# Performance work log

Hardware: AMD Instinct MI355X
Metric: run time of the kernel (lower is better)

The kernel has to match this reference:

```python
import jax, jax.numpy as jnp
import numpy as np

B, T, H, M, S, E, IN = 8, 2048, 64, 32, 20, 3, 32
EPS = 1e-8  # torch CosineSimilarity eps


def setup_inputs() -> dict:
    key = jax.random.key(0)
    ks = jax.random.split(key, 7)
    return {
        "x": jax.random.normal(ks[0], (B, T, IN), jnp.float32),
        "hidden": jax.random.normal(ks[1], (E, B, T, H), jnp.float32),
        "memory": jax.random.normal(ks[2], (S, M), jnp.float32),
        "Wq": jax.random.normal(ks[3], (E, H, M), jnp.float32),
        "Wk": jax.random.normal(ks[4], (E, H, M), jnp.float32),
        "Wv": jax.random.normal(ks[5], (E, H, M), jnp.float32),
        "input_query": jax.random.normal(ks[6], (IN, M), jnp.float32),
    }


def _cosine(a, b):
    # torch.nn.CosineSimilarity(dim=-1): each vector norm clamped to eps
    na = jnp.maximum(jnp.linalg.norm(a, axis=-1), EPS)
    nb = jnp.maximum(jnp.linalg.norm(b, axis=-1), EPS)
    return jnp.sum(a * b, axis=-1) / (na * nb)


def reference(x, hidden, memory, Wq, Wk, Wv, input_query):
    # query_mem: soft read from global memory slots
    q_in = jnp.einsum('bti,im->btm', x, input_query)           # [B,T,M]
    mem_sc = jax.nn.softmax(jnp.einsum('btm,sm->bts', q_in, memory), axis=-1)
    memories = jnp.einsum('bts,sm->btm', mem_sc, memory)       # [B,T,M]

    # per-expert tiny self-attention (vectorized over expert axis e)
    Q = jnp.einsum('ebth,ehm->ebtm', hidden, Wq)
    K = jnp.einsum('ebth,ehm->ebtm', hidden, Wk)
    V = jnp.einsum('ebth,ehm->ebtm', hidden, Wv)
    energy = jnp.einsum('ebtm,ebsm->ebts', Q, K)               # [E,B,T,T]
    att = jax.nn.softmax(energy, axis=-1)
    out = jnp.einsum('ebts,ebsm->ebtm', att, V)                # [E,B,T,M]

    cos = _cosine(memories[None], out)                         # [E,B,T]
    return jnp.moveaxis(cos, 0, -1)                            # [B,T,E]
```

## Files before the change

kernel.cpp:

```cpp
#include <hip/hip_runtime.h>
#include <hip/hip_bf16.h>

#define Bv  8
#define Tv  2048
#define Hv  64
#define Mv  32
#define Sv  20
#define Ev  3
#define INv 32
#define LOG2E 1.44269504088896340736f

typedef __attribute__((ext_vector_type(8))) _Float16 half8;
typedef __attribute__((ext_vector_type(2))) __fp16 fp16x2;
typedef __attribute__((ext_vector_type(4))) float float4v;

__global__ __launch_bounds__(256) void qkv_kernel(
    const float* __restrict__ hidden,
    const float* __restrict__ Wq,
    const float* __restrict__ Wk,
    const float* __restrict__ Wv,
    const float* __restrict__ x,
    const float* __restrict__ memory,
    const float* __restrict__ iq,
    _Float16* __restrict__ Qh, _Float16* __restrict__ Ql,
    _Float16* __restrict__ Kh, _Float16* __restrict__ Kl,
    _Float16* __restrict__ Vth,
    float* __restrict__ memout)
{
    __shared__ __align__(16) char qsm[43008];
    __shared__ float sIQ[32][32];
    __shared__ float sM[20][32];
    float* sHT = (float*)qsm;
    float* sW  = (float*)(qsm + 17408);

    int bid  = blockIdx.x;
    int tile = bid & 31;
    int b    = (bid >> 5) & 7;
    int e    = bid >> 8;
    int tid  = threadIdx.x;
    size_t eb = (size_t)(e * Bv + b);
    size_t row0 = eb * Tv + (size_t)tile * 64;
    const float* hbase = hidden + row0 * Hv;

    for (int i = tid; i < 32 * 32; i += 256) sIQ[i >> 5][i & 31] = iq[i];
    for (int i = tid; i < 20 * 32; i += 256) sM[i >> 5][i & 31] = memory[i];

    {
        int r  = tid >> 2;
        int c4 = tid & 3;
#pragma unroll
        for (int hh = 0; hh < 4; ++hh) {
            int h4 = c4 + hh * 4;
            float4 v = ((const float4*)(hbase + (size_t)r * Hv))[h4];
            sHT[(h4*4+0)*68 + r] = v.x; sHT[(h4*4+1)*68 + r] = v.y;
            sHT[(h4*4+2)*68 + r] = v.z; sHT[(h4*4+3)*68 + r] = v.w;
        }
    }
    {
        const float* wq = Wq + (size_t)e * Hv * Mv;
        const float* wk = Wk + (size_t)e * Hv * Mv;
        const float* wv = Wv + (size_t)e * Hv * Mv;
        for (int i = tid; i < Hv * Mv; i += 256) {
            int h = i >> 5, m = i & 31;
            sW[h*100 + m]      = wq[i];
            sW[h*100 + 32 + m] = wk[i];
            sW[h*100 + 64 + m] = wv[i];
        }
    }
    __syncthreads();

    int ty = tid >> 4, tx = tid & 15;
    float acc[4][6];
#pragma unroll
    for (int i = 0; i < 4; ++i)
#pragma unroll
        for (int j = 0; j < 6; ++j) acc[i][j] = 0.f;

    for (int h = 0; h < 64; ++h) {
        float4 av = *(const float4*)&sHT[h*68 + ty * 4];
        float a[4] = {av.x, av.y, av.z, av.w};
        float bb[6];
#pragma unroll
        for (int j = 0; j < 6; ++j) bb[j] = sW[h*100 + tx * 6 + j];
#pragma unroll
        for (int i = 0; i < 4; ++i)
#pragma unroll
            for (int j = 0; j < 6; ++j) acc[i][j] = fmaf(a[i], bb[j], acc[i][j]);
    }

    __syncthreads();
    char* sQh = qsm;
    char* sQl = qsm + 4096;
    char* sKh = qsm + 8192;
    char* sKl = qsm + 12288;
    char* sVh = qsm + 16384;
#pragma unroll
    for (int i = 0; i < 4; ++i) {
        int row = ty * 4 + i;
#pragma unroll
        for (int j = 0; j < 6; ++j) {
            int c = tx * 6 + j;
            float v = acc[i][j];
            if (c < 32) {
                v *= LOG2E;
                _Float16 h16 = (_Float16)v;
                _Float16 l16 = (_Float16)(v - (float)h16);
                *(_Float16*)(sQh + row * 64 + c * 2) = h16;
                *(_Float16*)(sQl + row * 64 + c * 2) = l16;
            } else if (c < 64) {
                _Float16 h16 = (_Float16)v;
                _Float16 l16 = (_Float16)(v - (float)h16);
                int m = c - 32, q = m >> 3, wi = m & 7;
                int off = row * 64 + (((q + row) & 3) << 4) + wi * 2;
                *(_Float16*)(sKh + off) = h16;
                *(_Float16*)(sKl + off) = l16;
            } else {
                int d = c - 64, c8 = row >> 3, wi = row & 7;
                int off = d * 128 + (((c8 + d) & 7) << 4) + wi * 2;
                *(_Float16*)(sVh + off) = (_Float16)v;
            }
        }
    }
    __syncthreads();

    size_t pb = eb * (size_t)Tv * 32 + (size_t)tile * 2048;
    _Float16* dsts[5] = {Qh + pb, Ql + pb, Kh + pb, Kl + pb, Vth + pb};
#pragma unroll
    for (int pl = 0; pl < 5; ++pl)
        ((float4*)dsts[pl])[tid] = ((const float4*)(qsm + pl * 4096))[tid];

    if (e == 0 && tid < 64) {
        int t = b * Tv + tile * 64 + tid;
        const float4* xr = (const float4*)(x + (size_t)t * INv);
        float xv[32];
#pragma unroll
        for (int i = 0; i < 8; ++i) {
            float4 v = xr[i];
            xv[4*i] = v.x; xv[4*i+1] = v.y; xv[4*i+2] = v.z; xv[4*i+3] = v.w;
        }
        float qm[32];
#pragma unroll
        for (int m = 0; m < 32; ++m) qm[m] = 0.f;
        for (int i = 0; i < 32; ++i) {
            float xi = xv[i];
#pragma unroll
            for (int m4 = 0; m4 < 8; ++m4) {
                float4 wv = *(const float4*)&sIQ[i][m4 * 4];
                qm[4*m4]   = fmaf(xi, wv.x, qm[4*m4]);
                qm[4*m4+1] = fmaf(xi, wv.y, qm[4*m4+1]);
                qm[4*m4+2] = fmaf(xi, wv.z, qm[4*m4+2]);
                qm[4*m4+3] = fmaf(xi, wv.w, qm[4*m4+3]);
            }
        }
        float sc[20];
#pragma unroll
        for (int j = 0; j < 20; ++j) {
            float a2 = 0.f;
#pragma unroll
            for (int m = 0; m < 32; ++m) a2 = fmaf(qm[m], sM[j][m], a2);
            sc[j] = a2;
        }
        float mx = sc[0];
#pragma unroll
        for (int j = 1; j < 20; ++j) mx = fmaxf(mx, sc[j]);
        float psum = 0.f, p[20];
#pragma unroll
        for (int j = 0; j < 20; ++j) { p[j] = exp2f((sc[j] - mx) * LOG2E); psum += p[j]; }
        float inv = 1.0f / psum;
        float mo[32];
#pragma unroll
        for (int m = 0; m < 32; ++m) mo[m] = 0.f;
        for (int j = 0; j < 20; ++j) {
            float pj = p[j];
#pragma unroll
            for (int m = 0; m < 32; ++m) mo[m] = fmaf(pj, sM[j][m], mo[m]);
        }
        float4* outp = (float4*)(memout + (size_t)t * Mv);
#pragma unroll
        for (int m4 = 0; m4 < 8; ++m4) {
            float4 v;
            v.x = mo[4*m4] * inv; v.y = mo[4*m4+1] * inv;
            v.z = mo[4*m4+2] * inv; v.w = mo[4*m4+3] * inv;
            outp[m4] = v;
        }
    }
}

__device__ __forceinline__ void load_lds16(const _Float16* g, char* l) {
    __builtin_amdgcn_global_load_lds(
        (const __attribute__((address_space(1))) void*)g,
        (__attribute__((address_space(3))) void*)l, 16, 0, 0);
}

__global__ __launch_bounds__(256, 1) void attn_kernel(
    const _Float16* __restrict__ Qh, const _Float16* __restrict__ Ql,
    const _Float16* __restrict__ Kh, const _Float16* __restrict__ Kl,
    const _Float16* __restrict__ Vth,
    const float* __restrict__ memv,
    float* __restrict__ out)
{
    __shared__ __align__(16) char smem[32768];
    const int PW = 24576;

    int bid  = blockIdx.x;
    int xcd  = bid & 7;
    int slot = bid >> 3;
    int tile = slot & 31;
    int ebi  = xcd + ((slot >> 5) << 3);
    int e    = ebi >> 3;
    int b    = ebi & 7;
    int tid  = threadIdx.x;
    int lane = tid & 63;
    int w    = tid >> 6;
    int quad = lane >> 4;
    int l15  = lane & 15;
    size_t eb = (size_t)ebi;
    int q0 = tile * 64 + w * 16;

    size_t qoff = (eb * Tv + (size_t)(q0 + l15)) * 32 + quad * 8;
    half8 qH = *(const half8*)(Qh + qoff);
    half8 qL = *(const half8*)(Ql + qoff);

    float4v O0 = {0.f, 0.f, 0.f, 0.f};
    float4v O1 = {0.f, 0.f, 0.f, 0.f};
    float m_run = -3.0e38f;

    size_t ebOff = eb * (size_t)Tv * 32;
    const _Float16* gp[3] = {Kh + ebOff, Kl + ebOff, Vth + ebOff};

#pragma unroll
    for (int j = 0; j < 3; ++j) {
        int idx = w * 3 + j, p = idx >> 2, k = idx & 3;
        load_lds16(gp[p] + (size_t)k * 512 + lane * 8,
                   smem + p * 4096 + k * 1024);
    }

    for (int c = 0; c < 32; ++c) {
        int pb = c & 1;
        __syncthreads();
        if (c + 1 < 32) {
#pragma unroll
            for (int j = 0; j < 3; ++j) {
                int idx = w * 3 + j, p = idx >> 2, k = idx & 3;
                load_lds16(gp[p] + (size_t)(c + 1) * 2048 + k * 512 + lane * 8,
                           smem + (pb ^ 1) * 12288 + p * 4096 + k * 1024);
            }
        }
        const char* base = smem + pb * 12288;

        float s[16];
        float cmax = -3.0e38f;
#pragma unroll
        for (int tau = 0; tau < 4; ++tau) {
            int r = tau * 16 + l15;
            int sw = ((quad + r) & 3) << 4;
            half8 aH = *(const half8*)(base + r * 64 + sw);
            half8 aL = *(const half8*)(base + 4096 + r * 64 + sw);
            float4v acc = {0.f, 0.f, 0.f, 0.f};
            acc = __builtin_amdgcn_mfma_f32_16x16x32_f16(aH, qL, acc, 0, 0, 0);
            acc = __builtin_amdgcn_mfma_f32_16x16x32_f16(aL, qH, acc, 0, 0, 0);
            acc = __builtin_amdgcn_mfma_f32_16x16x32_f16(aH, qH, acc, 0, 0, 0);
#pragma unroll
            for (int r2 = 0; r2 < 4; ++r2) {
                s[tau * 4 + r2] = acc[r2];
                cmax = fmaxf(cmax, acc[r2]);
            }
        }
        cmax = fmaxf(cmax, __shfl_xor(cmax, 16));
        cmax = fmaxf(cmax, __shfl_xor(cmax, 32));
        float mNew  = fmaxf(m_run, cmax);
        float alpha = exp2f(m_run - mNew);
#pragma unroll
        for (int i = 0; i < 16; ++i)
            s[i] = exp2f(s[i] - mNew);
        m_run = mNew;

#pragma unroll
        for (int r = 0; r < 4; ++r) {
            float ar = __shfl(alpha, quad * 4 + r, 16);
            O0[r] *= ar;
            O1[r] *= ar;
        }

        char* pw = smem + PW + w * 2048 + l15 * 128;
        int xr = l15 & 7;
#pragma unroll
        for (int tau = 0; tau < 4; ++tau) {
            fp16x2 h01 = __builtin_amdgcn_cvt_pkrtz(s[tau*4+0], s[tau*4+1]);
            fp16x2 h23 = __builtin_amdgcn_cvt_pkrtz(s[tau*4+2], s[tau*4+3]);
            uint2 u;
            u.x = __builtin_bit_cast(unsigned int, h01);
            u.y = __builtin_bit_cast(unsigned int, h23);
            int bi = tau * 2 + (quad >> 1);
            *(uint2*)(pw + ((bi ^ xr) << 4) + (quad & 1) * 8) = u;
        }
        __asm__ volatile("" ::: "memory");

#pragma unroll
        for (int ks = 0; ks < 2; ++ks) {
            int swv = ((ks * 4 + quad + l15) & 7) << 4;
            half8 pA  = *(const half8*)(pw + (((ks * 4 + quad) ^ xr) << 4));
            half8 v0H = *(const half8*)(base + 8192 + l15 * 128 + swv);
            half8 v1H = *(const half8*)(base + 8192 + (16 + l15) * 128 + swv);
            O0 = __builtin_amdgcn_mfma_f32_16x16x32_f16(pA, v0H, O0, 0, 0, 0);
            O1 = __builtin_amdgcn_mfma_f32_16x16x32_f16(pA, v1H, O1, 0, 0, 0);
        }
    }

    const float* mb = memv + (size_t)b * Tv * 32;
    float dotr[4], nor[4], nmr[4];
#pragma unroll
    for (int r = 0; r < 4; ++r) {
        int trow = q0 + quad * 4 + r;
        float mv0 = mb[(size_t)trow * 32 + l15];
        float mv1 = mb[(size_t)trow * 32 + 16 + l15];
        float d  = O0[r] * mv0 + O1[r] * mv1;
        float n  = O0[r] * O0[r] + O1[r] * O1[r];
        float nm = mv0 * mv0 + mv1 * mv1;
#pragma unroll
        for (int delta = 1; delta < 16; delta <<= 1) {
            d  += __shfl_xor(d,  delta);
            n  += __shfl_xor(n,  delta);
            nm += __shfl_xor(nm, delta);
        }
        dotr[r] = d; nor[r] = n; nmr[r] = nm;
    }
    if (l15 < 4) {
        int r = l15;
        float na = fmaxf(sqrtf(nmr[r]), 1e-8f);
        float nb = fmaxf(sqrtf(nor[r]), 1e-30f);
        float cosv = dotr[r] / (na * nb);
        int trow = q0 + quad * 4 + r;
        out[((size_t)b * Tv + trow) * Ev + e] = cosv;
    }
}

extern "C" void kernel_launch(void* const* d_in, const int* in_sizes, int n_in,
                              void* d_out, int out_size, void* d_ws, size_t ws_size,
                              hipStream_t stream) {
    const float* x      = (const float*)d_in[0];
    const float* hidden = (const float*)d_in[1];
    const float* memory = (const float*)d_in[2];
    const float* Wq     = (const float*)d_in[3];
    const float* Wk     = (const float*)d_in[4];
    const float* Wv     = (const float*)d_in[5];
    const float* iq     = (const float*)d_in[6];
    float* out          = (float*)d_out;

    char* ws = (char*)d_ws;
    const size_t PLANE = (size_t)Ev * Bv * Tv * 32 * 2;
    float*    memout = (float*)ws;
    _Float16* Qh  = (_Float16*)(ws + 2097152);
    _Float16* Ql  = (_Float16*)(ws + 2097152 + PLANE);
    _Float16* Kh  = (_Float16*)(ws + 2097152 + 2 * PLANE);
    _Float16* Kl  = (_Float16*)(ws + 2097152 + 3 * PLANE);
    _Float16* Vth = (_Float16*)(ws + 2097152 + 4 * PLANE);

    qkv_kernel<<<Ev * Bv * (Tv / 64), 256, 0, stream>>>(hidden, Wq, Wk, Wv,
                                                        x, memory, iq,
                                                        Qh, Ql, Kh, Kl, Vth, memout);
    attn_kernel<<<Ev * Bv * (Tv / 64), 256, 0, stream>>>(Qh, Ql, Kh, Kl, Vth,
                                                         memout, out);
}
```

Measured before the change: 148.6 us.

## Compute QKV projection with split-fp16 MFMA instead of scalar FMA

Replaces the scalar FP32 FMA loop in the QKV projection kernel with MFMA 16x16x32 fp16 instructions. Both the hidden rows and the weights are split into hi/lo fp16 parts, and three MFMAs per k-block approximate FP32 precision. Weights are pre-split into swizzled shared memory, the hidden transpose through LDS is removed, and the LOG2E scale is folded into the weights. It also loads the iq/memory tables only for expert 0 blocks. This shrinks shared memory and cuts ALU work in the projection stage, but it drops the lo*lo term, which adds small rounding error.

```diff
diff --git a/kernel.cpp b/kernel.cpp
--- a/kernel.cpp
+++ b/kernel.cpp
@@ -13,6 +13,16 @@
 typedef __attribute__((ext_vector_type(8))) _Float16 half8;
 typedef __attribute__((ext_vector_type(2))) __fp16 fp16x2;
 typedef __attribute__((ext_vector_type(4))) float float4v;
+
+__device__ __forceinline__ void split2x4(float4 a, float4 b, half8& h, half8& l) {
+    float vv[8] = {a.x, a.y, a.z, a.w, b.x, b.y, b.z, b.w};
+#pragma unroll
+    for (int i = 0; i < 8; ++i) {
+        _Float16 hh = (_Float16)vv[i];
+        h[i] = hh;
+        l[i] = (_Float16)(vv[i] - (float)hh);
+    }
+}
 
 __global__ __launch_bounds__(256) void qkv_kernel(
     const float* __restrict__ hidden,
@@ -27,93 +37,108 @@
     _Float16* __restrict__ Vth,
     float* __restrict__ memout)
 {
-    __shared__ __align__(16) char qsm[43008];
+    __shared__ __align__(16) char sBlob[24576];
     __shared__ float sIQ[32][32];
     __shared__ float sM[20][32];
-    float* sHT = (float*)qsm;
-    float* sW  = (float*)(qsm + 17408);
 
     int bid  = blockIdx.x;
     int tile = bid & 31;
     int b    = (bid >> 5) & 7;
     int e    = bid >> 8;
     int tid  = threadIdx.x;
+    int lane = tid & 63;
+    int w    = tid >> 6;
+    int quad = lane >> 4;
+    int l15  = lane & 15;
     size_t eb = (size_t)(e * Bv + b);
     size_t row0 = eb * Tv + (size_t)tile * 64;
     const float* hbase = hidden + row0 * Hv;
 
-    for (int i = tid; i < 32 * 32; i += 256) sIQ[i >> 5][i & 31] = iq[i];
-    for (int i = tid; i < 20 * 32; i += 256) sM[i >> 5][i & 31] = memory[i];
+    const float* arow = hbase + (size_t)(w * 16 + l15) * Hv + quad * 8;
+    float4 a0 = *(const float4*)(arow);
+    float4 a1 = *(const float4*)(arow + 4);
+    float4 a2 = *(const float4*)(arow + 32);
+    float4 a3 = *(const float4*)(arow + 36);
+
+    if (e == 0) {
+        for (int i = tid; i < 32 * 32; i += 256) sIQ[i >> 5][i & 31] = iq[i];
+        for (int i = tid; i < 20 * 32; i += 256) sM[i >> 5][i & 31] = memory[i];
+    }
 
     {
-        int r  = tid >> 2;
-        int c4 = tid & 3;
-#pragma unroll
-        for (int hh = 0; hh < 4; ++hh) {
-            int h4 = c4 + hh * 4;
-            float4 v = ((const float4*)(hbase + (size_t)r * Hv))[h4];
-            sHT[(h4*4+0)*68 + r] = v.x; sHT[(h4*4+1)*68 + r] = v.y;
-            sHT[(h4*4+2)*68 + r] = v.z; sHT[(h4*4+3)*68 + r] = v.w;
-        }
-    }
-    {
-        const float* wq = Wq + (size_t)e * Hv * Mv;
-        const float* wk = Wk + (size_t)e * Hv * Mv;
-        const float* wv = Wv + (size_t)e * Hv * Mv;
-        for (int i = tid; i < Hv * Mv; i += 256) {
-            int h = i >> 5, m = i & 31;
-            sW[h*100 + m]      = wq[i];
-            sW[h*100 + 32 + m] = wk[i];
-            sW[h*100 + 64 + m] = wv[i];
-        }
-    }
+        const float* wsrc[3] = {Wq + (size_t)e * Hv * Mv,
+                                Wk + (size_t)e * Hv * Mv,
+                                Wv + (size_t)e * Hv * Mv};
+#pragma unroll
+        for (int j = 0; j < 3; ++j) {
+            int u  = tid + j * 256;
+            int c  = u >> 3, kb = u & 7;
+            const float* src = wsrc[c >> 5] + (c & 31);
+            float scale = (c < 32) ? LOG2E : 1.f;
+            half8 hi, lo;
+#pragma unroll
+            for (int i = 0; i < 8; ++i) {
+                float v = src[(kb * 8 + i) * Mv] * scale;
+                _Float16 hh = (_Float16)v;
+                hi[i] = hh;
+                lo[i] = (_Float16)(v - (float)hh);
+            }
+            int off = c * 128 + ((kb ^ (c & 7)) << 4);
+            *(half8*)(sBlob + off)         = hi;
+            *(half8*)(sBlob + 12288 + off) = lo;
+        }
+    }
+
+    half8 aH0, aL0, aH1, aL1;
+    split2x4(a0, a1, aH0, aL0);
+    split2x4(a2, a3, aH1, aL1);
+
     __syncthreads();
 
-    int ty = tid >> 4, tx = tid & 15;
-    float acc[4][6];
-#pragma unroll
-    for (int i = 0; i < 4; ++i)
-#pragma unroll
-        for (int j = 0; j < 6; ++j) acc[i][j] = 0.f;
-
-    for (int h = 0; h < 64; ++h) {
-        float4 av = *(const float4*)&sHT[h*68 + ty * 4];
-        float a[4] = {av.x, av.y, av.z, av.w};
-        float bb[6];
-#pragma unroll
-        for (int j = 0; j < 6; ++j) bb[j] = sW[h*100 + tx * 6 + j];
-#pragma unroll
-        for (int i = 0; i < 4; ++i)
-#pragma unroll
-            for (int j = 0; j < 6; ++j) acc[i][j] = fmaf(a[i], bb[j], acc[i][j]);
+    float4v accs[6];
+    int x7 = l15 & 7;
+#pragma unroll
+    for (int ct = 0; ct < 6; ++ct) {
+        const char* brow = sBlob + (ct * 16 + l15) * 128;
+        half8 bH0 = *(const half8*)(brow + ((quad ^ x7) << 4));
+        half8 bH1 = *(const half8*)(brow + (((4 + quad) ^ x7) << 4));
+        half8 bL0 = *(const half8*)(brow + 12288 + ((quad ^ x7) << 4));
+        half8 bL1 = *(const half8*)(brow + 12288 + (((4 + quad) ^ x7) << 4));
+        float4v acc = {0.f, 0.f, 0.f, 0.f};
+        acc = __builtin_amdgcn_mfma_f32_16x16x32_f16(aH0, bL0, acc, 0, 0, 0);
+        acc = __builtin_amdgcn_mfma_f32_16x16x32_f16(aL0, bH0, acc, 0, 0, 0);
+        acc = __builtin_amdgcn_mfma_f32_16x16x32_f16(aH0, bH0, acc, 0, 0, 0);
+        acc = __builtin_amdgcn_mfma_f32_16x16x32_f16(aH1, bL1, acc, 0, 0, 0);
+        acc = __builtin_amdgcn_mfma_f32_16x16x32_f16(aL1, bH1, acc, 0, 0, 0);
+        acc = __builtin_amdgcn_mfma_f32_16x16x32_f16(aH1, bH1, acc, 0, 0, 0);
+        accs[ct] = acc;
     }
 
     __syncthreads();
-    char* sQh = qsm;
-    char* sQl = qsm + 4096;
-    char* sKh = qsm + 8192;
-    char* sKl = qsm + 12288;
-    char* sVh = qsm + 16384;
-#pragma unroll
-    for (int i = 0; i < 4; ++i) {
-        int row = ty * 4 + i;
-#pragma unroll
-        for (int j = 0; j < 6; ++j) {
-            int c = tx * 6 + j;
-            float v = acc[i][j];
-            if (c < 32) {
-                v *= LOG2E;
+
+    char* sQh = sBlob;
+    char* sQl = sBlob + 4096;
+    char* sKh = sBlob + 8192;
+    char* sKl = sBlob + 12288;
+    char* sVh = sBlob + 16384;
+    int rbase = w * 16 + quad * 4;
+#pragma unroll
+    for (int ct = 0; ct < 6; ++ct) {
+        int c = ct * 16 + l15;
+#pragma unroll
+        for (int r = 0; r < 4; ++r) {
+            int row = rbase + r;
+            float v = accs[ct][r];
+            if (ct < 2) {
                 _Float16 h16 = (_Float16)v;
-                _Float16 l16 = (_Float16)(v - (float)h16);
                 *(_Float16*)(sQh + row * 64 + c * 2) = h16;
-                *(_Float16*)(sQl + row * 64 + c * 2) = l16;
-            } else if (c < 64) {
+                *(_Float16*)(sQl + row * 64 + c * 2) = (_Float16)(v - (float)h16);
+            } else if (ct < 4) {
                 _Float16 h16 = (_Float16)v;
-                _Float16 l16 = (_Float16)(v - (float)h16);
                 int m = c - 32, q = m >> 3, wi = m & 7;
                 int off = row * 64 + (((q + row) & 3) << 4) + wi * 2;
                 *(_Float16*)(sKh + off) = h16;
-                *(_Float16*)(sKl + off) = l16;
+                *(_Float16*)(sKl + off) = (_Float16)(v - (float)h16);
             } else {
                 int d = c - 64, c8 = row >> 3, wi = row & 7;
                 int off = d * 128 + (((c8 + d) & 7) << 4) + wi * 2;
@@ -127,7 +152,7 @@
     _Float16* dsts[5] = {Qh + pb, Ql + pb, Kh + pb, Kl + pb, Vth + pb};
 #pragma unroll
     for (int pl = 0; pl < 5; ++pl)
-        ((float4*)dsts[pl])[tid] = ((const float4*)(qsm + pl * 4096))[tid];
+        ((float4*)dsts[pl])[tid] = ((const float4*)(sBlob + pl * 4096))[tid];
 
     if (e == 0 && tid < 64) {
         int t = b * Tv + tile * 64 + tid;
```

New measurement: 146.0 us. No clear change (-1.7%).
